# Kernel optimization log

Hardware: AMD Instinct MI355X
Metric: run time of the kernel (lower is better)

Reference implementation:

```python
import jax, jax.numpy as jnp
import numpy as np

N_NODES = 50000
N_EDGES = 600000
D_IN = 128
D_OUT = 128
N_BASES = 4
N_RATINGS = 5


def setup_inputs() -> dict:
    key = jax.random.key(0)
    k1, k2, k3, k4, k5, k6 = jax.random.split(key, 6)
    x = jax.random.normal(k1, (N_NODES, D_IN), dtype=jnp.float32)
    edge_index = jax.random.randint(k2, (2, N_EDGES), 0, N_NODES, dtype=jnp.int64)
    edge_type = jax.random.randint(k3, (N_EDGES,), 0, N_RATINGS, dtype=jnp.int64)
    # basis matrices B_k: (out, in); a_r stacked over ratings: (R, K); W_0: (out, in)
    B = jax.random.normal(k4, (N_BASES, D_OUT, D_IN), dtype=jnp.float32) * 0.05
    A = jax.random.normal(k5, (N_RATINGS, N_BASES), dtype=jnp.float32) * 0.05
    W0 = jax.random.normal(k6, (D_OUT, D_IN), dtype=jnp.float32) * 0.05
    return {"x": x, "edge_index": edge_index, "edge_type": edge_type, "B": B, "A": A, "W0": W0}


def reference(x, edge_index, edge_type, B, A, W0):
    # self-loop term: (W0 @ x^T)^T == x @ W0^T
    n_nodes = x.shape[0]
    src, tgt = edge_index[0], edge_index[1]
    out = x @ W0.T  # [N, out]
    # per-relation basis-composed weights W_r = sum_k a_r[k] * B_k  -> [R, out, in]
    W = jnp.einsum('rk,kod->rod', A, B)
    n_ratings = A.shape[0]
    for r in range(n_ratings):  # small fixed relation set
        h = x @ W[r].T                     # [N, out] transform once per node
        msg = jnp.where((edge_type == r)[:, None], h[src], jnp.float32(0))  # [E, out]
        out = out + jax.ops.segment_sum(msg, tgt, num_segments=n_nodes)
    return out
```

## Files before the change

kernel.cpp:

```cpp
#include <hip/hip_runtime.h>

#define N_NODES 50000
#define N_EDGES 600000
#define D 128
#define KTOT 768
#define NB_SCAN 196

typedef __attribute__((ext_vector_type(8))) short short8;
typedef __attribute__((ext_vector_type(4))) float float4v;

static __device__ __forceinline__ float bf2f(unsigned int u16) {
    union { unsigned int i; float f; } v; v.i = u16 << 16; return v.f;
}
static __device__ __forceinline__ unsigned short f2bf(float f) {
    union { float f; unsigned int i; } v; v.f = f;
    unsigned int u = v.i;
    return (unsigned short)((u + 0x7FFFu + ((u >> 16) & 1u)) >> 16);
}
static __device__ __forceinline__ float h2f(unsigned int h) {
    unsigned int s = (h >> 15) & 1u, e = (h >> 10) & 0x1fu, m = h & 0x3ffu;
    unsigned int bits = (e == 0) ? (s << 31)
                                 : ((s << 31) | ((e + 112u) << 23) | (m << 13));
    union { unsigned int i; float f; } v; v.i = bits; return v.f;
}

__global__ __launch_bounds__(256) void setup(int* __restrict__ flags,
                                             int* __restrict__ cnt) {
    int i = blockIdx.x * 256 + threadIdx.x;
    if (i < N_NODES) cnt[i] = 0;
    if (i < 8) flags[i] = 0;
}

__global__ __launch_bounds__(256) void detect_all(const int* __restrict__ ei,
                                                  const int* __restrict__ et,
                                                  const unsigned int* __restrict__ x,
                                                  const unsigned int* __restrict__ B,
                                                  const unsigned int* __restrict__ A,
                                                  const unsigned int* __restrict__ W0,
                                                  int* __restrict__ flags) {
    __shared__ int sflag;
    if (threadIdx.x == 0) sflag = 0;
    __syncthreads();
    int b = blockIdx.x, acc = 0, fidx;
    if (b < 64) {
        fidx = 0;
        for (int i = b * 256 + threadIdx.x; i < N_EDGES; i += 64 * 256)
            acc |= ei[2 * i + 1];
    } else if (b < 80) {
        fidx = 1;
        for (int i = (b - 64) * 256 + threadIdx.x; i < N_EDGES / 2; i += 16 * 256)
            acc |= et[2 * i + 1];
    } else if (b < 96) {
        fidx = 2;
        for (int i = (b - 80) * 256 + threadIdx.x; i < 600000; i += 16 * 256) {
            unsigned int e = (x[i] >> 7) & 0xffu;
            acc |= (e > 0xA0u || e < 0x50u) ? 1 : 0;
        }
    } else if (b < 100) {
        fidx = 3;
        for (int i = (b - 96) * 256 + threadIdx.x; i < 32768; i += 4 * 256) {
            unsigned int e = (B[i] >> 7) & 0xffu;
            acc |= (e > 0xA0u || e < 0x50u) ? 1 : 0;
        }
    } else if (b == 100) {
        fidx = 4;
        for (int i = threadIdx.x; i < 10; i += 256) {
            unsigned int e = (A[i] >> 7) & 0xffu;
            acc |= (e > 0xA0u || e < 0x50u) ? 1 : 0;
        }
    } else if (b < 103) {
        fidx = 5;
        for (int i = (b - 101) * 256 + threadIdx.x; i < 8192; i += 2 * 256) {
            unsigned int e = (W0[i] >> 7) & 0xffu;
            acc |= (e > 0xA0u || e < 0x50u) ? 1 : 0;
        }
    } else {
        fidx = 6;
        for (int i = (b - 103) * 256 + threadIdx.x; i < 300000; i += 16 * 256) {
            unsigned int el = (x[i] >> 7) & 0xffu, eh = (x[i] >> 23) & 0xffu;
            acc |= (el < 0x58u || eh < 0x58u) ? 1 : 0;
        }
    }
    if (acc) sflag = 1;
    __syncthreads();
    if (threadIdx.x == 0 && sflag) atomicOr(flags + fidx, 1);
}

__global__ __launch_bounds__(256) void norm_hist(const int* __restrict__ ei,
                                                 const int* __restrict__ et,
                                                 int* __restrict__ idx32,
                                                 int* __restrict__ et32,
                                                 int* __restrict__ cnt,
                                                 const int* __restrict__ flags) {
    int b = blockIdx.x;
    if (b < 4688) {
        int i = b * 256 + threadIdx.x;
        if (i < 2 * N_EDGES) {
            int v = flags[0] ? ei[i] : ei[2 * i];
            idx32[i] = v;
            if (i >= N_EDGES && (unsigned)v < (unsigned)N_NODES)
                atomicAdd(&cnt[v], 1);
        }
    } else {
        int i = (b - 4688) * 256 + threadIdx.x;
        if (i < N_EDGES) et32[i] = flags[1] ? et[i] : et[2 * i];
    }
}

static __device__ __forceinline__ float loadw(const void* p, int idx, int f32) {
    return f32 ? ((const float*)p)[idx] : bf2f(((const unsigned short*)p)[idx]);
}

__global__ __launch_bounds__(256) void prep_wB(const void* __restrict__ A,
                                               const void* __restrict__ B,
                                               const void* __restrict__ W0,
                                               unsigned short* __restrict__ wcatB,
                                               const int* __restrict__ flags) {
    int idx = blockIdx.x * 256 + threadIdx.x;
    int fB = flags[3], fA = flags[4], fW = flags[5];
    int o = idx / KTOT, k = idx % KTOT;
    float v;
    if (k < D) {
        v = loadw(W0, o * D + k, fW);
    } else {
        int r = (k - D) >> 7, d = (k - D) & 127;
        v = 0.f;
#pragma unroll
        for (int j = 0; j < 4; ++j)
            v += loadw(A, r * 4 + j, fA) * loadw(B, (j * D + o) * D + d, fB);
    }
    wcatB[idx] = f2bf(v);
}

__global__ __launch_bounds__(256) void prep_wt6_direct(const void* __restrict__ A,
                                                       const void* __restrict__ B,
                                                       const void* __restrict__ W0,
                                                       float* __restrict__ wcatT6F,
                                                       const int* __restrict__ flags) {
    int idx = blockIdx.x * 256 + threadIdx.x;
    int fB = flags[3], fA = flags[4], fW = flags[5];
    int slot = idx >> 14, d = (idx >> 7) & 127, o = idx & 127;
    float v;
    if (slot == 0) {
        v = loadw(W0, o * D + d, fW);
    } else {
        int r = slot - 1;
        v = 0.f;
#pragma unroll
        for (int j = 0; j < 4; ++j)
            v += loadw(A, r * 4 + j, fA) * loadw(B, (j * D + o) * D + d, fB);
    }
    wcatT6F[idx] = v;
}

__global__ __launch_bounds__(256) void scan1(const int* __restrict__ cnt,
                                             int* __restrict__ bsum) {
    __shared__ int sh[256];
    int t = threadIdx.x, idx = blockIdx.x * 256 + t;
    sh[t] = (idx < N_NODES) ? cnt[idx] : 0;
    __syncthreads();
    for (int off = 128; off > 0; off >>= 1) {
        if (t < off) sh[t] += sh[t + off];
        __syncthreads();
    }
    if (t == 0) bsum[blockIdx.x] = sh[0];
}

__global__ __launch_bounds__(64) void scan2(const int* __restrict__ bsum,
                                            int* __restrict__ bscan,
                                            int* __restrict__ offsets) {
    if (threadIdx.x != 0) return;
    int run = 0;
    for (int b = 0; b < NB_SCAN; ++b) { bscan[b] = run; run += bsum[b]; }
    offsets[N_NODES] = run;
}

__global__ __launch_bounds__(256) void scan3(const int* __restrict__ cnt,
                                             const int* __restrict__ bscan,
                                             int* __restrict__ offsets,
                                             int* __restrict__ cursor) {
    __shared__ int sh[256];
    int t = threadIdx.x, idx = blockIdx.x * 256 + t;
    int v = (idx < N_NODES) ? cnt[idx] : 0;
    sh[t] = v;
    __syncthreads();
    for (int off = 1; off < 256; off <<= 1) {
        int a = (t >= off) ? sh[t - off] : 0;
        __syncthreads();
        sh[t] += a;
        __syncthreads();
    }
    if (idx < N_NODES) {
        int excl = sh[t] - v + bscan[blockIdx.x];
        offsets[idx] = excl;
        cursor[idx] = excl;
    }
}

__global__ __launch_bounds__(256) void place(const int* __restrict__ src,
                                             const int* __restrict__ tgt,
                                             const int* __restrict__ et,
                                             int* __restrict__ cursor,
                                             int* __restrict__ entries) {
    int e = blockIdx.x * 256 + threadIdx.x;
    if (e >= N_EDGES) return;
    int s = src[e], g = tgt[e], r = et[e];
    if ((unsigned)s >= (unsigned)N_NODES || (unsigned)g >= (unsigned)N_NODES || (unsigned)r >= 5u) return;
    int pos = atomicAdd(&cursor[g], 1);
    entries[pos] = s * 8 + r;
}

__global__ __launch_bounds__(256) void conv_x(const void* __restrict__ xraw,
                                              unsigned short* __restrict__ Xcat,
                                              const int* __restrict__ flags) {
    int idx = blockIdx.x * 256 + threadIdx.x;
    int n = idx >> 5, cg = idx & 31;
    int f32 = flags[2], f16 = flags[6];
    unsigned short o0, o1, o2, o3;
    if (f32) {
        float4 v = *((const float4*)xraw + idx);
        o0 = f2bf(v.x); o1 = f2bf(v.y); o2 = f2bf(v.z); o3 = f2bf(v.w);
    } else {
        uint2 v = *((const uint2*)xraw + idx);
        if (f16) {
            o0 = f2bf(h2f(v.x & 0xffffu)); o1 = f2bf(h2f(v.x >> 16));
            o2 = f2bf(h2f(v.y & 0xffffu)); o3 = f2bf(h2f(v.y >> 16));
        } else {
            o0 = v.x & 0xffffu; o1 = v.x >> 16; o2 = v.y & 0xffffu; o3 = v.y >> 16;
        }
    }
    unsigned long long pack = (unsigned long long)o0 | ((unsigned long long)o1 << 16) |
                              ((unsigned long long)o2 << 32) | ((unsigned long long)o3 << 48);
    *(unsigned long long*)(Xcat + (size_t)n * KTOT + cg * 4) = pack;
}

#define AGG_ACC(xw)                                            \
    {                                                          \
        int r = ent & 7;                                       \
        float lo = bf2f((xw) & 0xffffu), hi = bf2f((xw) >> 16);\
        if (r == 0)      { a0 += lo; a1 += hi; }               \
        else if (r == 1) { b0 += lo; b1 += hi; }               \
        else if (r == 2) { c0 += lo; c1 += hi; }               \
        else if (r == 3) { d0 += lo; d1 += hi; }               \
        else             { e0 += lo; e1 += hi; }               \
    }

__global__ __launch_bounds__(256) void aggregate(const int* __restrict__ offsets,
                                                 const int* __restrict__ entries,
                                                 unsigned int* __restrict__ Xcat32) {
    __shared__ float part[4][5][130];
    int tid = threadIdx.x;
    int wid = tid >> 6, lane = tid & 63;
    int slot = wid >> 1;
    int half = wid & 1;
    int n = blockIdx.x * 2 + slot;
    int beg = offsets[n], end = offsets[n + 1];
    int mid = (beg + end + 1) >> 1;
    int lo = half ? mid : beg, hi = half ? end : mid;
    float a0 = 0, a1 = 0, b0 = 0, b1 = 0, c0 = 0, c1 = 0, d0 = 0, d1 = 0, e0 = 0, e1 = 0;

    int i = lo;
    for (; i + 3 < hi; i += 4) {
        int en0 = entries[i], en1 = entries[i + 1], en2 = entries[i + 2], en3 = entries[i + 3];
        unsigned int s0 = (unsigned)(en0 >> 3) < (unsigned)N_NODES ? (unsigned)(en0 >> 3) : 0u;
        unsigned int s1 = (unsigned)(en1 >> 3) < (unsigned)N_NODES ? (unsigned)(en1 >> 3) : 0u;
        unsigned int s2 = (unsigned)(en2 >> 3) < (unsigned)N_NODES ? (unsigned)(en2 >> 3) : 0u;
        unsigned int s3 = (unsigned)(en3 >> 3) < (unsigned)N_NODES ? (unsigned)(en3 >> 3) : 0u;
        unsigned int x0 = Xcat32[(size_t)s0 * 384 + lane];
        unsigned int x1 = Xcat32[(size_t)s1 * 384 + lane];
        unsigned int x2 = Xcat32[(size_t)s2 * 384 + lane];
        unsigned int x3 = Xcat32[(size_t)s3 * 384 + lane];
        { int ent = en0; AGG_ACC(x0); }
        { int ent = en1; AGG_ACC(x1); }
        { int ent = en2; AGG_ACC(x2); }
        { int ent = en3; AGG_ACC(x3); }
    }
    for (; i < hi; ++i) {
        int ent = entries[i];
        unsigned int s = (unsigned)(ent >> 3) < (unsigned)N_NODES ? (unsigned)(ent >> 3) : 0u;
        unsigned int xw = Xcat32[(size_t)s * 384 + lane];
        AGG_ACC(xw);
    }

    part[wid][0][2 * lane] = a0; part[wid][0][2 * lane + 1] = a1;
    part[wid][1][2 * lane] = b0; part[wid][1][2 * lane + 1] = b1;
    part[wid][2][2 * lane] = c0; part[wid][2][2 * lane + 1] = c1;
    part[wid][3][2 * lane] = d0; part[wid][3][2 * lane + 1] = d1;
    part[wid][4][2 * lane] = e0; part[wid][4][2 * lane + 1] = e1;
    __syncthreads();

    for (int u = tid; u < 640; u += 256) {
        int s = u / 320, rem = u % 320;
        int r = rem >> 6, c = rem & 63;
        float lo2 = part[2 * s][r][2 * c]     + part[2 * s + 1][r][2 * c];
        float hi2 = part[2 * s][r][2 * c + 1] + part[2 * s + 1][r][2 * c + 1];
        Xcat32[(size_t)(blockIdx.x * 2 + s) * 384 + 64 + r * 64 + c] =
            (unsigned int)f2bf(lo2) | ((unsigned int)f2bf(hi2) << 16);
    }
}

__global__ __launch_bounds__(256) void gemm_mfma(const unsigned short* __restrict__ Xcat,
                                                 const unsigned short* __restrict__ wcatB,
                                                 float* __restrict__ outF) {
    __shared__ unsigned short xs[128 * 72];
    __shared__ unsigned short wsd[128 * 72];
    int tid = threadIdx.x;
    int m0 = blockIdx.x * 128;
    int wid = tid >> 6, lane = tid & 63;
    int wm = (wid & 1) * 64, wn = (wid >> 1) * 64;
    int lm = lane & 15, kg = lane >> 4;

    float4v accf[4][4];
#pragma unroll
    for (int i = 0; i < 4; ++i)
#pragma unroll
        for (int j = 0; j < 4; ++j) accf[i][j] = (float4v){0.f, 0.f, 0.f, 0.f};

    for (int kc = 0; kc < 12; ++kc) {
        if (kc) __syncthreads();
#pragma unroll
        for (int i = 0; i < 4; ++i) {
            int c = tid + i * 256;
            int row = c >> 3;
            int col = (c & 7) * 8;
            int gm = m0 + row;
            short8 xv = {0, 0, 0, 0, 0, 0, 0, 0};
            if (gm < N_NODES)
                xv = *(const short8*)(Xcat + (size_t)gm * KTOT + kc * 64 + col);
            *(short8*)(&xs[row * 72 + col]) = xv;
            short8 wv = *(const short8*)(wcatB + (size_t)row * KTOT + kc * 64 + col);
            *(short8*)(&wsd[row * 72 + col]) = wv;
        }
        __syncthreads();
#pragma unroll
        for (int kb = 0; kb < 2; ++kb) {
            int k = kb * 32 + kg * 8;
            short8 a[4], b[4];
#pragma unroll
            for (int i = 0; i < 4; ++i)
                a[i] = *(const short8*)(&xs[(wm + i * 16 + lm) * 72 + k]);
#pragma unroll
            for (int i = 0; i < 4; ++i)
                b[i] = *(const short8*)(&wsd[(wn + i * 16 + lm) * 72 + k]);
#pragma unroll
            for (int i = 0; i < 4; ++i)
#pragma unroll
                for (int j = 0; j < 4; ++j)
                    accf[i][j] = __builtin_amdgcn_mfma_f32_16x16x32_bf16(a[i], b[j], accf[i][j], 0, 0, 0);
        }
    }

#pragma unroll
    for (int i = 0; i < 4; ++i) {
        int gmb = m0 + wm + i * 16 + kg * 4;
#pragma unroll
        for (int j = 0; j < 4; ++j) {
            int gn = wn + j * 16 + lm;
#pragma unroll
            for (int r = 0; r < 4; ++r) {
                int gm = gmb + r;
                if (gm < N_NODES) outF[(size_t)gm * D + gn] = accf[i][j][r];
            }
        }
    }
}

static __device__ __forceinline__ float2 readx2(const void* x, int node, int lane,
                                                int f32, int f16) {
    if (f32) return *((const float2*)x + (size_t)node * 64 + lane);
    unsigned int w = *((const unsigned int*)x + (size_t)node * 64 + lane);
    float2 r;
    if (f16) { r.x = h2f(w & 0xffffu); r.y = h2f(w >> 16); }
    else     { r.x = bf2f(w & 0xffffu); r.y = bf2f(w >> 16); }
    return r;
}

__global__ __launch_bounds__(256) void self_raw(const void* __restrict__ x,
                                                const float* __restrict__ wcatT6F,
                                                float* __restrict__ outF,
                                                const int* __restrict__ flags) {
    int t = blockIdx.x * 256 + threadIdx.x;
    int n = t >> 6, lane = t & 63;
    int f32 = flags[2], f16 = flags[6];
    float2 xp = readx2(x, n, lane, f32, f16);
    float m0 = 0.f, m1 = 0.f;
#pragma unroll 8
    for (int dp = 0; dp < 64; ++dp) {
        float xa = __shfl(xp.x, dp);
        float xc = __shfl(xp.y, dp);
        float2 w0 = *(const float2*)(wcatT6F + (size_t)(2 * dp) * D + 2 * lane);
        float2 w1 = *(const float2*)(wcatT6F + (size_t)(2 * dp + 1) * D + 2 * lane);
        m0 += xa * w0.x + xc * w1.x;
        m1 += xa * w0.y + xc * w1.y;
    }
    *((float2*)outF + (size_t)n * 64 + lane) = make_float2(m0, m1);
}

__global__ __launch_bounds__(256) void edge_raw(const int* __restrict__ src,
                                                const int* __restrict__ tgt,
                                                const int* __restrict__ et,
                                                const void* __restrict__ x,
                                                const float* __restrict__ wcatT6F,
                                                float* __restrict__ outF,
                                                const int* __restrict__ flags) {
    int t = blockIdx.x * 256 + threadIdx.x;
    int e = t >> 6, lane = t & 63;
    if (e >= N_EDGES) return;
    int f32 = flags[2], f16 = flags[6];
    int s = src[e], g = tgt[e], r = et[e];
    if ((unsigned)s >= (unsigned)N_NODES || (unsigned)g >= (unsigned)N_NODES || (unsigned)r >= 5u) return;
    float2 xp = readx2(x, s, lane, f32, f16);
    const float* wt = wcatT6F + (size_t)(1 + r) * D * D;
    float m0 = 0.f, m1 = 0.f;
#pragma unroll 8
    for (int dp = 0; dp < 64; ++dp) {
        float xa = __shfl(xp.x, dp);
        float xc = __shfl(xp.y, dp);
        float2 w0 = *(const float2*)(wt + (size_t)(2 * dp) * D + 2 * lane);
        float2 w1 = *(const float2*)(wt + (size_t)(2 * dp + 1) * D + 2 * lane);
        m0 += xa * w0.x + xc * w1.x;
        m1 += xa * w0.y + xc * w1.y;
    }
    float* ap = outF + (size_t)g * D + lane * 2;
    atomicAdd(ap + 0, m0);
    atomicAdd(ap + 1, m1);
}

extern "C" void kernel_launch(void* const* d_in, const int* in_sizes, int n_in,
                              void* d_out, int out_size, void* d_ws, size_t ws_size,
                              hipStream_t stream) {
    const void* x  = nullptr; const int* ei = nullptr; const int* et = nullptr;
    const void* B  = nullptr; const void* A = nullptr; const void* W0 = nullptr;
    for (int i = 0; i < n_in; ++i) {
        switch (in_sizes[i]) {
            case 6400000: x  = d_in[i]; break;
            case 1200000: ei = (const int*)d_in[i]; break;
            case 600000:  et = (const int*)d_in[i]; break;
            case 65536:   B  = d_in[i]; break;
            case 20:      A  = d_in[i]; break;
            case 16384:   W0 = d_in[i]; break;
            default: break;
        }
    }
    if (!x || !ei || !et || !B || !A || !W0) {
        x  = d_in[0]; ei = (const int*)d_in[1]; et = (const int*)d_in[2];
        B  = d_in[3]; A  = d_in[4]; W0 = d_in[5];
    }
    float* outF = (float*)d_out;

    char* ws = (char*)d_ws;
    int*   flags   = (int*)(ws + 0);
    float* wcatT6F = (float*)(ws + 256);
    unsigned short* wcatB = (unsigned short*)(ws + 393472);
    int* offsets  = (int*)(ws + 590080);
    int* cursor   = (int*)(ws + 790144);
    int* cnt      = (int*)(ws + 990144);
    int* bsum     = (int*)(ws + 1190144);
    int* bscan    = (int*)(ws + 1191168);
    int* entries  = (int*)(ws + 1192192);
    int* idx32    = (int*)(ws + 3592192);
    int* et32     = (int*)(ws + 8392192);
    unsigned short* Xcat = (unsigned short*)(ws + 3592192);
    const size_t needMain = 3592192ull + 76800000ull;
    const size_t needT3   = 393472ull;

    int* src32 = idx32;
    int* tgt32 = idx32 + N_EDGES;

    setup<<<NB_SCAN, 256, 0, stream>>>(flags, cnt);
    detect_all<<<119, 256, 0, stream>>>(ei, et, (const unsigned int*)x,
                                        (const unsigned int*)B, (const unsigned int*)A,
                                        (const unsigned int*)W0, flags);

    if (ws_size >= needMain) {
        prep_wB<<<384, 256, 0, stream>>>(A, B, W0, wcatB, flags);
        norm_hist<<<7032, 256, 0, stream>>>(ei, et, idx32, et32, cnt, flags);
        scan1<<<NB_SCAN, 256, 0, stream>>>(cnt, bsum);
        scan2<<<1, 64, 0, stream>>>(bsum, bscan, offsets);
        scan3<<<NB_SCAN, 256, 0, stream>>>(cnt, bscan, offsets, cursor);
        place<<<2344, 256, 0, stream>>>(src32, tgt32, et32, cursor, entries);
        conv_x<<<6250, 256, 0, stream>>>(x, Xcat, flags);
        aggregate<<<25000, 256, 0, stream>>>(offsets, entries, (unsigned int*)Xcat);
        gemm_mfma<<<391, 256, 0, stream>>>(Xcat, wcatB, outF);
    } else if (ws_size >= needT3) {
        prep_wt6_direct<<<384, 256, 0, stream>>>(A, B, W0, wcatT6F, flags);
        self_raw<<<12500, 256, 0, stream>>>(x, wcatT6F, outF, flags);
        edge_raw<<<150000, 256, 0, stream>>>(ei, ei + N_EDGES, et, x, wcatT6F, outF, flags);
    }
}
```

Baseline: 280.0 us.

## Fuse weight prep into hist kernel, shuffle-broadcast edge entries, halve GEMM tile

Folds the prep_wB weight-composition kernel into the norm_hist launch as extra blocks, removing one kernel launch. In aggregate, each wave now loads up to 64 edge entries with one coalesced load and broadcasts them with __shfl, instead of every lane re-reading the same entries. The GEMM M-tile drops from 128 to 64 rows, doubling the grid from 391 to 782 blocks so more CUs have work, at the cost of reloading the weight tile twice as often.

```diff
diff --git a/kernel.cpp b/kernel.cpp
--- a/kernel.cpp
+++ b/kernel.cpp
@@ -86,12 +86,20 @@
     if (threadIdx.x == 0 && sflag) atomicOr(flags + fidx, 1);
 }
 
-__global__ __launch_bounds__(256) void norm_hist(const int* __restrict__ ei,
-                                                 const int* __restrict__ et,
-                                                 int* __restrict__ idx32,
-                                                 int* __restrict__ et32,
-                                                 int* __restrict__ cnt,
-                                                 const int* __restrict__ flags) {
+static __device__ __forceinline__ float loadw(const void* p, int idx, int f32) {
+    return f32 ? ((const float*)p)[idx] : bf2f(((const unsigned short*)p)[idx]);
+}
+
+__global__ __launch_bounds__(256) void norm_hist_prep(const int* __restrict__ ei,
+                                                      const int* __restrict__ et,
+                                                      int* __restrict__ idx32,
+                                                      int* __restrict__ et32,
+                                                      int* __restrict__ cnt,
+                                                      const void* __restrict__ A,
+                                                      const void* __restrict__ B,
+                                                      const void* __restrict__ W0,
+                                                      unsigned short* __restrict__ wcatB,
+                                                      const int* __restrict__ flags) {
     int b = blockIdx.x;
     if (b < 4688) {
         int i = b * 256 + threadIdx.x;
@@ -101,35 +109,25 @@
             if (i >= N_EDGES && (unsigned)v < (unsigned)N_NODES)
                 atomicAdd(&cnt[v], 1);
         }
-    } else {
+    } else if (b < 7032) {
         int i = (b - 4688) * 256 + threadIdx.x;
         if (i < N_EDGES) et32[i] = flags[1] ? et[i] : et[2 * i];
-    }
-}
-
-static __device__ __forceinline__ float loadw(const void* p, int idx, int f32) {
-    return f32 ? ((const float*)p)[idx] : bf2f(((const unsigned short*)p)[idx]);
-}
-
-__global__ __launch_bounds__(256) void prep_wB(const void* __restrict__ A,
-                                               const void* __restrict__ B,
-                                               const void* __restrict__ W0,
-                                               unsigned short* __restrict__ wcatB,
-                                               const int* __restrict__ flags) {
-    int idx = blockIdx.x * 256 + threadIdx.x;
-    int fB = flags[3], fA = flags[4], fW = flags[5];
-    int o = idx / KTOT, k = idx % KTOT;
-    float v;
-    if (k < D) {
-        v = loadw(W0, o * D + k, fW);
     } else {
-        int r = (k - D) >> 7, d = (k - D) & 127;
-        v = 0.f;
-#pragma unroll
-        for (int j = 0; j < 4; ++j)
-            v += loadw(A, r * 4 + j, fA) * loadw(B, (j * D + o) * D + d, fB);
-    }
-    wcatB[idx] = f2bf(v);
+        int idx = (b - 7032) * 256 + threadIdx.x;
+        int fB = flags[3], fA = flags[4], fW = flags[5];
+        int o = idx / KTOT, k = idx % KTOT;
+        float v;
+        if (k < D) {
+            v = loadw(W0, o * D + k, fW);
+        } else {
+            int r = (k - D) >> 7, d = (k - D) & 127;
+            v = 0.f;
+#pragma unroll
+            for (int j = 0; j < 4; ++j)
+                v += loadw(A, r * 4 + j, fA) * loadw(B, (j * D + o) * D + d, fB);
+        }
+        wcatB[idx] = f2bf(v);
+    }
 }
 
 __global__ __launch_bounds__(256) void prep_wt6_direct(const void* __restrict__ A,
@@ -237,13 +235,15 @@
 #define AGG_ACC(xw)                                            \
     {                                                          \
         int r = ent & 7;                                       \
-        float lo = bf2f((xw) & 0xffffu), hi = bf2f((xw) >> 16);\
-        if (r == 0)      { a0 += lo; a1 += hi; }               \
-        else if (r == 1) { b0 += lo; b1 += hi; }               \
-        else if (r == 2) { c0 += lo; c1 += hi; }               \
-        else if (r == 3) { d0 += lo; d1 += hi; }               \
-        else             { e0 += lo; e1 += hi; }               \
-    }
+        float flo = bf2f((xw) & 0xffffu), fhi = bf2f((xw) >> 16);\
+        if (r == 0)      { a0 += flo; a1 += fhi; }             \
+        else if (r == 1) { b0 += flo; b1 += fhi; }             \
+        else if (r == 2) { c0 += flo; c1 += fhi; }             \
+        else if (r == 3) { d0 += flo; d1 += fhi; }             \
+        else             { e0 += flo; e1 += fhi; }             \
+    }
+
+#define AGG_GATHER(en) Xcat32[(size_t)((unsigned)((en) >> 3) < (unsigned)N_NODES ? (unsigned)((en) >> 3) : 0u) * 384 + lane]
 
 __global__ __launch_bounds__(256) void aggregate(const int* __restrict__ offsets,
                                                  const int* __restrict__ entries,
@@ -259,27 +259,29 @@
     int lo = half ? mid : beg, hi = half ? end : mid;
     float a0 = 0, a1 = 0, b0 = 0, b1 = 0, c0 = 0, c1 = 0, d0 = 0, d1 = 0, e0 = 0, e1 = 0;
 
-    int i = lo;
-    for (; i + 3 < hi; i += 4) {
-        int en0 = entries[i], en1 = entries[i + 1], en2 = entries[i + 2], en3 = entries[i + 3];
-        unsigned int s0 = (unsigned)(en0 >> 3) < (unsigned)N_NODES ? (unsigned)(en0 >> 3) : 0u;
-        unsigned int s1 = (unsigned)(en1 >> 3) < (unsigned)N_NODES ? (unsigned)(en1 >> 3) : 0u;
-        unsigned int s2 = (unsigned)(en2 >> 3) < (unsigned)N_NODES ? (unsigned)(en2 >> 3) : 0u;
-        unsigned int s3 = (unsigned)(en3 >> 3) < (unsigned)N_NODES ? (unsigned)(en3 >> 3) : 0u;
-        unsigned int x0 = Xcat32[(size_t)s0 * 384 + lane];
-        unsigned int x1 = Xcat32[(size_t)s1 * 384 + lane];
-        unsigned int x2 = Xcat32[(size_t)s2 * 384 + lane];
-        unsigned int x3 = Xcat32[(size_t)s3 * 384 + lane];
-        { int ent = en0; AGG_ACC(x0); }
-        { int ent = en1; AGG_ACC(x1); }
-        { int ent = en2; AGG_ACC(x2); }
-        { int ent = en3; AGG_ACC(x3); }
-    }
-    for (; i < hi; ++i) {
-        int ent = entries[i];
-        unsigned int s = (unsigned)(ent >> 3) < (unsigned)N_NODES ? (unsigned)(ent >> 3) : 0u;
-        unsigned int xw = Xcat32[(size_t)s * 384 + lane];
-        AGG_ACC(xw);
+    for (int base = lo; base < hi; base += 64) {
+        int navail = hi - base;
+        int cnt = navail < 64 ? navail : 64;
+        int eidx = base + (lane < cnt ? lane : cnt - 1);
+        int eload = entries[eidx];
+        int j = 0;
+        for (; j + 3 < cnt; j += 4) {
+            int en0 = __shfl(eload, j), en1 = __shfl(eload, j + 1);
+            int en2 = __shfl(eload, j + 2), en3 = __shfl(eload, j + 3);
+            unsigned int x0 = AGG_GATHER(en0);
+            unsigned int x1 = AGG_GATHER(en1);
+            unsigned int x2 = AGG_GATHER(en2);
+            unsigned int x3 = AGG_GATHER(en3);
+            { int ent = en0; AGG_ACC(x0); }
+            { int ent = en1; AGG_ACC(x1); }
+            { int ent = en2; AGG_ACC(x2); }
+            { int ent = en3; AGG_ACC(x3); }
+        }
+        for (; j < cnt; ++j) {
+            int ent = __shfl(eload, j);
+            unsigned int xw = AGG_GATHER(ent);
+            AGG_ACC(xw);
+        }
     }
 
     part[wid][0][2 * lane] = a0; part[wid][0][2 * lane + 1] = a1;
@@ -302,32 +304,36 @@
 __global__ __launch_bounds__(256) void gemm_mfma(const unsigned short* __restrict__ Xcat,
                                                  const unsigned short* __restrict__ wcatB,
                                                  float* __restrict__ outF) {
-    __shared__ unsigned short xs[128 * 72];
+    __shared__ unsigned short xs[64 * 72];
     __shared__ unsigned short wsd[128 * 72];
     int tid = threadIdx.x;
-    int m0 = blockIdx.x * 128;
+    int m0 = blockIdx.x * 64;
     int wid = tid >> 6, lane = tid & 63;
-    int wm = (wid & 1) * 64, wn = (wid >> 1) * 64;
+    int wm = (wid & 1) * 32, wn = (wid >> 1) * 64;
     int lm = lane & 15, kg = lane >> 4;
 
-    float4v accf[4][4];
-#pragma unroll
-    for (int i = 0; i < 4; ++i)
+    float4v accf[2][4];
+#pragma unroll
+    for (int i = 0; i < 2; ++i)
 #pragma unroll
         for (int j = 0; j < 4; ++j) accf[i][j] = (float4v){0.f, 0.f, 0.f, 0.f};
 
     for (int kc = 0; kc < 12; ++kc) {
         if (kc) __syncthreads();
 #pragma unroll
-        for (int i = 0; i < 4; ++i) {
+        for (int i = 0; i < 2; ++i) {
             int c = tid + i * 256;
-            int row = c >> 3;
-            int col = (c & 7) * 8;
+            int row = c >> 3, col = (c & 7) * 8;
             int gm = m0 + row;
             short8 xv = {0, 0, 0, 0, 0, 0, 0, 0};
             if (gm < N_NODES)
                 xv = *(const short8*)(Xcat + (size_t)gm * KTOT + kc * 64 + col);
             *(short8*)(&xs[row * 72 + col]) = xv;
+        }
+#pragma unroll
+        for (int i = 0; i < 4; ++i) {
+            int c = tid + i * 256;
+            int row = c >> 3, col = (c & 7) * 8;
             short8 wv = *(const short8*)(wcatB + (size_t)row * KTOT + kc * 64 + col);
             *(short8*)(&wsd[row * 72 + col]) = wv;
         }
@@ -335,15 +341,15 @@
 #pragma unroll
         for (int kb = 0; kb < 2; ++kb) {
             int k = kb * 32 + kg * 8;
-            short8 a[4], b[4];
-#pragma unroll
-            for (int i = 0; i < 4; ++i)
+            short8 a[2], b[4];
+#pragma unroll
+            for (int i = 0; i < 2; ++i)
                 a[i] = *(const short8*)(&xs[(wm + i * 16 + lm) * 72 + k]);
 #pragma unroll
-            for (int i = 0; i < 4; ++i)
-                b[i] = *(const short8*)(&wsd[(wn + i * 16 + lm) * 72 + k]);
-#pragma unroll
-            for (int i = 0; i < 4; ++i)
+            for (int j = 0; j < 4; ++j)
+                b[j] = *(const short8*)(&wsd[(wn + j * 16 + lm) * 72 + k]);
+#pragma unroll
+            for (int i = 0; i < 2; ++i)
 #pragma unroll
                 for (int j = 0; j < 4; ++j)
                     accf[i][j] = __builtin_amdgcn_mfma_f32_16x16x32_bf16(a[i], b[j], accf[i][j], 0, 0, 0);
@@ -351,7 +357,7 @@
     }
 
 #pragma unroll
-    for (int i = 0; i < 4; ++i) {
+    for (int i = 0; i < 2; ++i) {
         int gmb = m0 + wm + i * 16 + kg * 4;
 #pragma unroll
         for (int j = 0; j < 4; ++j) {
@@ -473,15 +479,15 @@
                                         (const unsigned int*)W0, flags);
 
     if (ws_size >= needMain) {
-        prep_wB<<<384, 256, 0, stream>>>(A, B, W0, wcatB, flags);
-        norm_hist<<<7032, 256, 0, stream>>>(ei, et, idx32, et32, cnt, flags);
+        norm_hist_prep<<<7416, 256, 0, stream>>>(ei, et, idx32, et32, cnt,
+                                                 A, B, W0, wcatB, flags);
         scan1<<<NB_SCAN, 256, 0, stream>>>(cnt, bsum);
         scan2<<<1, 64, 0, stream>>>(bsum, bscan, offsets);
         scan3<<<NB_SCAN, 256, 0, stream>>>(cnt, bscan, offsets, cursor);
         place<<<2344, 256, 0, stream>>>(src32, tgt32, et32, cursor, entries);
         conv_x<<<6250, 256, 0, stream>>>(x, Xcat, flags);
         aggregate<<<25000, 256, 0, stream>>>(offsets, entries, (unsigned int*)Xcat);
-        gemm_mfma<<<391, 256, 0, stream>>>(Xcat, wcatB, outF);
+        gemm_mfma<<<782, 256, 0, stream>>>(Xcat, wcatB, outF);
     } else if (ws_size >= needT3) {
         prep_wt6_direct<<<384, 256, 0, stream>>>(A, B, W0, wcatT6F, flags);
         self_raw<<<12500, 256, 0, stream>>>(x, wcatT6F, outF, flags);
```

Result: faster. 260.6 us (-6.9%).
